# Kernel tuning notes

Measured on AMD Instinct MI355X. Metric: run time of the kernel, lower is better.

Reference implementation:

```python
import jax, jax.numpy as jnp
import numpy as np

N = 16384
INPUT_DIM = 256
HIDDEN1 = 128
HIDDEN2 = 64


def setup_inputs() -> dict:
    key = jax.random.key(0)
    ks = jax.random.split(key, 8)
    X = jax.random.normal(ks[0], (N, INPUT_DIM), dtype=jnp.float32)
    adj = jax.random.uniform(ks[1], (N, N), dtype=jnp.float32)
    # Xavier-uniform style scaling for weights
    def xavier(k, shape):
        fan_in, fan_out = shape
        lim = float(np.sqrt(6.0 / (fan_in + fan_out)))
        return jax.random.uniform(k, shape, dtype=jnp.float32, minval=-lim, maxval=lim)
    W1 = xavier(ks[2], (INPUT_DIM, HIDDEN1))
    Wm = xavier(ks[3], (HIDDEN1, HIDDEN2))
    Ws = xavier(ks[4], (HIDDEN1, HIDDEN2))
    Wp = xavier(ks[5], (HIDDEN2, HIDDEN2))
    bp = jnp.zeros((HIDDEN2,), dtype=jnp.float32)
    noise = jax.random.normal(ks[6], (N, HIDDEN2), dtype=jnp.float32)
    return {"X": X, "adj": adj, "W1": W1, "Wm": Wm, "Ws": Ws,
            "Wp": Wp, "bp": bp, "noise": noise}


def _gcn(x, adj, W, activation):
    # GraphConvSparse: adj @ (x @ W) then activation
    h = adj @ (x @ W)
    return activation(h)


def reference(X, adj, W1, Wm, Ws, Wp, bp, noise):
    # base GCN with ReLU
    hidden = _gcn(X, adj, W1, jax.nn.relu)            # [N, hidden1]
    # mean branch: identity-activation GCN then Linear projection
    Z = _gcn(hidden, adj, Wm, lambda x: x)            # [N, hidden2]
    mean = Z @ Wp + bp                                # [N, hidden2]
    # logstd branch with clamp(max=10)
    logstd = _gcn(hidden, adj, Ws, lambda x: x)
    logstd = jnp.minimum(logstd, 10.0)
    # reparameterization trick
    sampled_z = noise * jnp.exp(logstd) + mean        # [N, hidden2]
    return sampled_z
```

## Files before the change

kernel.cpp:

```cpp
#include <hip/hip_runtime.h>


typedef __bf16 bf16_t;
typedef __attribute__((ext_vector_type(8))) __bf16 bf16x8;
typedef __attribute__((ext_vector_type(16))) float f32x16;
typedef __attribute__((ext_vector_type(4)))  float f32x4;

#define N_NODES 16384

__device__ __forceinline__ int frag_off(int r, int c) {
    int K16  = r >> 4;
    int cblk = c >> 5;
    int g    = (r >> 3) & 1;
    int lane = (c & 31) + (g << 5);
    return ((K16 * 4 + cblk) << 9) + (lane << 3) + (r & 7);
}

template<int K, bool FUSED>
__global__ __launch_bounds__(256)
void producer_kernel(const float* __restrict__ A,
                     const float* __restrict__ W,
                     const float* __restrict__ Wa,
                     const float* __restrict__ Wb,
                     bf16_t* __restrict__ Bh,
                     bf16_t* __restrict__ Bl)
{
    __shared__ float As[32][128];
    __shared__ float Wsh[32][128];
    const int t    = threadIdx.x;
    const int row0 = blockIdx.x * 128;
    const int tc   = t & 15, tr = t >> 4;

    float acc[8][8];
    #pragma unroll
    for (int i = 0; i < 8; ++i)
        #pragma unroll
        for (int j = 0; j < 8; ++j) acc[i][j] = 0.f;

    const int ra = t >> 1, ks = (t & 1) << 4;
    const int wk = t >> 3, wc = (t & 7) << 4;

    for (int k0 = 0; k0 < K; k0 += 32) {
        const float* ap = A + (size_t)(row0 + ra) * K + k0 + ks;
        float4 a0 = *(const float4*)(ap);
        float4 a1 = *(const float4*)(ap + 4);
        float4 a2 = *(const float4*)(ap + 8);
        float4 a3 = *(const float4*)(ap + 12);
        float4 w0, w1, w2, w3;
        if (!FUSED) {
            const float* wp = W + (size_t)(k0 + wk) * 128 + wc;
            w0 = *(const float4*)(wp);     w1 = *(const float4*)(wp + 4);
            w2 = *(const float4*)(wp + 8); w3 = *(const float4*)(wp + 12);
        } else {
            const float* wp = (wc < 64) ? (Wa + (size_t)(k0 + wk) * 64 + wc)
                                        : (Wb + (size_t)(k0 + wk) * 64 + (wc - 64));
            w0 = *(const float4*)(wp);     w1 = *(const float4*)(wp + 4);
            w2 = *(const float4*)(wp + 8); w3 = *(const float4*)(wp + 12);
        }
        __syncthreads();
        {
            float tmp[16] = {a0.x,a0.y,a0.z,a0.w, a1.x,a1.y,a1.z,a1.w,
                             a2.x,a2.y,a2.z,a2.w, a3.x,a3.y,a3.z,a3.w};
            #pragma unroll
            for (int j = 0; j < 16; ++j) As[ks + j][ra] = tmp[j];
            *(float4*)&Wsh[wk][wc     ] = w0;
            *(float4*)&Wsh[wk][wc +  4] = w1;
            *(float4*)&Wsh[wk][wc +  8] = w2;
            *(float4*)&Wsh[wk][wc + 12] = w3;
        }
        __syncthreads();
        #pragma unroll 4
        for (int k = 0; k < 32; ++k) {
            float av[8], wv[8];
            *(float4*)&av[0] = *(const float4*)&As[k][8 * tr];
            *(float4*)&av[4] = *(const float4*)&As[k][8 * tr + 4];
            *(float4*)&wv[0] = *(const float4*)&Wsh[k][8 * tc];
            *(float4*)&wv[4] = *(const float4*)&Wsh[k][8 * tc + 4];
            #pragma unroll
            for (int i = 0; i < 8; ++i)
                #pragma unroll
                for (int j = 0; j < 8; ++j)
                    acc[i][j] = fmaf(av[i], wv[j], acc[i][j]);
        }
    }

    #pragma unroll
    for (int i = 0; i < 8; ++i) {
        int r = row0 + 8 * tr + i;
        #pragma unroll
        for (int j = 0; j < 8; ++j) {
            int c = 8 * tc + j;
            float v = acc[i][j];
            bf16_t h = (bf16_t)v;
            bf16_t l = (bf16_t)(v - (float)h);
            int off = frag_off(r, c);
            Bh[off] = h;
            Bl[off] = l;
        }
    }
}

template<int ACT>
__global__ __launch_bounds__(512, 2)
void adj_gemm_kernel(const float* __restrict__ adj,
                     const bf16_t* __restrict__ Bh,
                     const bf16_t* __restrict__ Bl,
                     float* __restrict__ out)
{
    __shared__ __align__(16) bf16_t AsH[2][64 * 64];
    __shared__ __align__(16) bf16_t AsL[2][64 * 64];
    const int t    = threadIdx.x;
    const int lane = t & 63;
    const int w    = t >> 6;
    const int wr   = w >> 2, wc = w & 3;
    const int row0 = blockIdx.x * 64;

    const int sr = t >> 3;
    const int sk = (t & 7) << 3;
    const float* aptr = adj + (size_t)(row0 + sr) * 16384 + sk;
    const int widx = ((sr << 6) + sk) ^ ((sr & 7) << 3);
    bf16_t* const wH0 = &AsH[0][widx]; bf16_t* const wH1 = &AsH[1][widx];
    bf16_t* const wL0 = &AsL[0][widx]; bf16_t* const wL1 = &AsL[1][widx];

    const int frow = (wr << 5) + (lane & 31);
    const int fg   = (lane >> 5) << 3;
    int ridx[4];
    #pragma unroll
    for (int s = 0; s < 4; ++s)
        ridx[s] = ((frow << 6) + (s << 4) + fg) ^ ((frow & 7) << 3);

    const int tb = (wc << 9) + (lane << 3);

    f32x16 acc;
    #pragma unroll
    for (int i = 0; i < 16; ++i) acc[i] = 0.f;

    auto loadB = [&](bf16x8* bh, bf16x8* bl, int step) {
        const size_t base = ((size_t)step << 13) + tb;
        #pragma unroll
        for (int s = 0; s < 4; ++s) {
            bh[s] = *(const bf16x8*)(Bh + base + (s << 11));
            bl[s] = *(const bf16x8*)(Bl + base + (s << 11));
        }
    };
    auto loadA = [&](f32x4& p0, f32x4& p1, int step) {
        const f32x4* p = (const f32x4*)(aptr + (step << 6));
        p0 = __builtin_nontemporal_load(p);
        p1 = __builtin_nontemporal_load(p + 1);
    };
    auto cvtWrite = [&](const f32x4& p0, const f32x4& p1, int buf) {
        float xs[8] = {p0[0], p0[1], p0[2], p0[3], p1[0], p1[1], p1[2], p1[3]};
        bf16x8 hv, lv;
        #pragma unroll
        for (int i = 0; i < 8; ++i) {
            bf16_t h = (bf16_t)xs[i];
            hv[i] = h;
            lv[i] = (bf16_t)(xs[i] - (float)h);
        }
        *(bf16x8*)(buf ? wH1 : wH0) = hv;
        *(bf16x8*)(buf ? wL1 : wL0) = lv;
    };
    auto compute = [&](int buf, const bf16x8* bh, const bf16x8* bl) {
        #pragma unroll
        for (int s = 0; s < 4; ++s) {
            const bf16_t* baseH = buf ? &AsH[1][0] : &AsH[0][0];
            const bf16_t* baseL = buf ? &AsL[1][0] : &AsL[0][0];
            bf16x8 ah = *(const bf16x8*)(baseH + ridx[s]);
            bf16x8 al = *(const bf16x8*)(baseL + ridx[s]);
            acc = __builtin_amdgcn_mfma_f32_32x32x16_bf16(ah, bh[s], acc, 0, 0, 0);
            acc = __builtin_amdgcn_mfma_f32_32x32x16_bf16(ah, bl[s], acc, 0, 0, 0);
            acc = __builtin_amdgcn_mfma_f32_32x32x16_bf16(al, bh[s], acc, 0, 0, 0);
        }
    };

#define SYNC_LDS() do { asm volatile("s_waitcnt lgkmcnt(0)" ::: "memory"); \
                        __builtin_amdgcn_s_barrier(); } while (0)

    f32x4 paA[4], paB[4];
    bf16x8 bhS0[4], blS0[4], bhS1[4], blS1[4];
    bf16x8 bhS2[4], blS2[4], bhS3[4], blS3[4];

    loadA(paA[0], paB[0], 0);
    loadA(paA[1], paB[1], 1);
    loadA(paA[2], paB[2], 2);
    loadA(paA[3], paB[3], 3);
    loadB(bhS0, blS0, 0);
    loadB(bhS1, blS1, 1);
    cvtWrite(paA[0], paB[0], 0);
    SYNC_LDS();

#define BODY(k, CH, CL, PH, PL) do {                                        \
        loadB(PH, PL, i0 + (k) + 2);                                        \
        loadA(paA[(k)], paB[(k)], i0 + (k) + 4);                            \
        compute((k) & 1, CH, CL);                                           \
        cvtWrite(paA[((k) + 1) & 3], paB[((k) + 1) & 3], ((k) + 1) & 1);    \
        SYNC_LDS();                                                         \
    } while (0)

    for (int i0 = 0; i0 < 252; i0 += 4) {
        BODY(0, bhS0, blS0, bhS2, blS2);
        BODY(1, bhS1, blS1, bhS3, blS3);
        BODY(2, bhS2, blS2, bhS0, blS0);
        BODY(3, bhS3, blS3, bhS1, blS1);
    }
#undef BODY

    loadB(bhS2, blS2, 254);
    compute(0, bhS0, blS0);
    cvtWrite(paA[1], paB[1], 1);
    SYNC_LDS();
    loadB(bhS3, blS3, 255);
    compute(1, bhS1, blS1);
    cvtWrite(paA[2], paB[2], 0);
    SYNC_LDS();
    compute(0, bhS2, blS2);
    cvtWrite(paA[3], paB[3], 1);
    SYNC_LDS();
    compute(1, bhS3, blS3);
#undef SYNC_LDS

    const int col = (wc << 5) + (lane & 31);
    const int rb  = row0 + (wr << 5) + ((lane >> 5) << 2);
    #pragma unroll
    for (int q = 0; q < 16; ++q) {
        int r = rb + (q & 3) + ((q >> 2) << 3);
        float v = acc[q];
        if (ACT == 1) v = fmaxf(v, 0.f);
        out[(size_t)r * 128 + col] = v;
    }
}

__global__ __launch_bounds__(256)
void final_kernel(const float* __restrict__ T,
                  const float* __restrict__ Wp,
                  const float* __restrict__ bp,
                  const float* __restrict__ noise,
                  float* __restrict__ out)
{
    __shared__ float Wps[64][64];
    __shared__ float Ts[64][64];
    const int t = threadIdx.x;
    const int row0 = blockIdx.x * 64;
    {
        int k = t >> 2, c0 = (t & 3) << 4;
        #pragma unroll
        for (int i = 0; i < 4; ++i)
            *(float4*)&Wps[k][c0 + 4 * i] = *(const float4*)&Wp[(size_t)k * 64 + c0 + 4 * i];
        #pragma unroll
        for (int i = 0; i < 4; ++i)
            *(float4*)&Ts[k][c0 + 4 * i] =
                *(const float4*)&T[(size_t)(row0 + k) * 128 + c0 + 4 * i];
    }
    __syncthreads();

    const int r  = t >> 2;
    const int c0 = (t & 3) << 4;
    float acc[16];
    #pragma unroll
    for (int j = 0; j < 16; ++j) acc[j] = bp[c0 + j];
    for (int k = 0; k < 64; ++k) {
        float a = Ts[r][k];
        #pragma unroll
        for (int j = 0; j < 16; ++j) acc[j] = fmaf(a, Wps[k][c0 + j], acc[j]);
    }
    const int grow = row0 + r;
    #pragma unroll
    for (int j = 0; j < 16; ++j) {
        float ls = T[(size_t)grow * 128 + 64 + c0 + j];
        ls = fminf(ls, 10.0f);
        out[(size_t)grow * 64 + c0 + j] =
            noise[(size_t)grow * 64 + c0 + j] * __expf(ls) + acc[j];
    }
}

extern "C" void kernel_launch(void* const* d_in, const int* in_sizes, int n_in,
                              void* d_out, int out_size, void* d_ws, size_t ws_size,
                              hipStream_t stream) {
    const float* X     = (const float*)d_in[0];
    const float* adj   = (const float*)d_in[1];
    const float* W1    = (const float*)d_in[2];
    const float* Wm    = (const float*)d_in[3];
    const float* Wsv   = (const float*)d_in[4];
    const float* Wp    = (const float*)d_in[5];
    const float* bp    = (const float*)d_in[6];
    const float* noise = (const float*)d_in[7];
    float* out = (float*)d_out;

    char* ws = (char*)d_ws;
    bf16_t* Bh   = (bf16_t*)ws;
    bf16_t* Bl   = (bf16_t*)(ws + (4u << 20));
    float*  Htmp = (float*)(ws + (8u << 20));

    producer_kernel<256, false><<<128, 256, 0, stream>>>(X, W1, nullptr, nullptr, Bh, Bl);
    adj_gemm_kernel<1><<<256, 512, 0, stream>>>(adj, Bh, Bl, Htmp);
    producer_kernel<128, true><<<128, 256, 0, stream>>>(Htmp, nullptr, Wm, Wsv, Bh, Bl);
    adj_gemm_kernel<0><<<256, 512, 0, stream>>>(adj, Bh, Bl, Htmp);
    final_kernel<<<256, 256, 0, stream>>>(Htmp, Wp, bp, noise, out);
}
```

Measured before the change: 783.1 us.

## Widen adjacency LDS tile to 256 K and cut barriers per tile

```diff
diff --git a/kernel.cpp b/kernel.cpp
--- a/kernel.cpp
+++ b/kernel.cpp
@@ -2,6 +2,7 @@
 
 
 typedef __bf16 bf16_t;
+typedef __attribute__((ext_vector_type(4))) __bf16 bf16x4;
 typedef __attribute__((ext_vector_type(8))) __bf16 bf16x8;
 typedef __attribute__((ext_vector_type(16))) float f32x16;
 typedef __attribute__((ext_vector_type(4)))  float f32x4;
@@ -107,27 +108,20 @@
                      const bf16_t* __restrict__ Bl,
                      float* __restrict__ out)
 {
-    __shared__ __align__(16) bf16_t AsH[2][64 * 64];
-    __shared__ __align__(16) bf16_t AsL[2][64 * 64];
+    __shared__ __align__(16) bf16_t AsH[2][64 * 256];
+    __shared__ __align__(16) bf16_t AsL[2][64 * 256];
     const int t    = threadIdx.x;
     const int lane = t & 63;
     const int w    = t >> 6;
     const int wr   = w >> 2, wc = w & 3;
     const int row0 = blockIdx.x * 64;
 
-    const int sr = t >> 3;
-    const int sk = (t & 7) << 3;
-    const float* aptr = adj + (size_t)(row0 + sr) * 16384 + sk;
-    const int widx = ((sr << 6) + sk) ^ ((sr & 7) << 3);
-    bf16_t* const wH0 = &AsH[0][widx]; bf16_t* const wH1 = &AsH[1][widx];
-    bf16_t* const wL0 = &AsL[0][widx]; bf16_t* const wL1 = &AsL[1][widx];
+    const float* aBase = adj + (size_t)(row0 + w * 8) * 16384 + lane * 4;
 
     const int frow = (wr << 5) + (lane & 31);
     const int fg   = (lane >> 5) << 3;
-    int ridx[4];
-    #pragma unroll
-    for (int s = 0; s < 4; ++s)
-        ridx[s] = ((frow << 6) + (s << 4) + fg) ^ ((frow & 7) << 3);
+    const int rswz = (frow & 7) << 3;
+    const int rbase = frow << 8;
 
     const int tb = (wc << 9) + (lane << 3);
 
@@ -135,38 +129,49 @@
     #pragma unroll
     for (int i = 0; i < 16; ++i) acc[i] = 0.f;
 
-    auto loadB = [&](bf16x8* bh, bf16x8* bl, int step) {
-        const size_t base = ((size_t)step << 13) + tb;
+    f32x4 ar[8];
+
+    auto loadAdj = [&](int mac) {
+        const float* p = aBase + (mac << 8);
+        ar[0] = __builtin_nontemporal_load((const f32x4*)(p));
+        ar[1] = __builtin_nontemporal_load((const f32x4*)(p + 16384));
+        ar[2] = __builtin_nontemporal_load((const f32x4*)(p + 2 * 16384));
+        ar[3] = __builtin_nontemporal_load((const f32x4*)(p + 3 * 16384));
+        ar[4] = __builtin_nontemporal_load((const f32x4*)(p + 4 * 16384));
+        ar[5] = __builtin_nontemporal_load((const f32x4*)(p + 5 * 16384));
+        ar[6] = __builtin_nontemporal_load((const f32x4*)(p + 6 * 16384));
+        ar[7] = __builtin_nontemporal_load((const f32x4*)(p + 7 * 16384));
+    };
+    auto cvtWrite = [&](int buf) {
+        #pragma unroll
+        for (int j = 0; j < 8; ++j) {
+            bf16x4 hv, lv;
+            #pragma unroll
+            for (int e = 0; e < 4; ++e) {
+                float v = ar[j][e];
+                bf16_t h = (bf16_t)v;
+                hv[e] = h;
+                lv[e] = (bf16_t)(v - (float)h);
+            }
+            int idx = (((w << 3) + j) << 8) + ((lane << 2) ^ (j << 3));
+            *(bf16x4*)&AsH[buf][idx] = hv;
+            *(bf16x4*)&AsL[buf][idx] = lv;
+        }
+    };
+    auto loadB = [&](bf16x8* bh, bf16x8* bl, int sub) {
+        const size_t base = ((size_t)sub << 13) + tb;
         #pragma unroll
         for (int s = 0; s < 4; ++s) {
             bh[s] = *(const bf16x8*)(Bh + base + (s << 11));
             bl[s] = *(const bf16x8*)(Bl + base + (s << 11));
         }
     };
-    auto loadA = [&](f32x4& p0, f32x4& p1, int step) {
-        const f32x4* p = (const f32x4*)(aptr + (step << 6));
-        p0 = __builtin_nontemporal_load(p);
-        p1 = __builtin_nontemporal_load(p + 1);
-    };
-    auto cvtWrite = [&](const f32x4& p0, const f32x4& p1, int buf) {
-        float xs[8] = {p0[0], p0[1], p0[2], p0[3], p1[0], p1[1], p1[2], p1[3]};
-        bf16x8 hv, lv;
-        #pragma unroll
-        for (int i = 0; i < 8; ++i) {
-            bf16_t h = (bf16_t)xs[i];
-            hv[i] = h;
-            lv[i] = (bf16_t)(xs[i] - (float)h);
-        }
-        *(bf16x8*)(buf ? wH1 : wH0) = hv;
-        *(bf16x8*)(buf ? wL1 : wL0) = lv;
-    };
-    auto compute = [&](int buf, const bf16x8* bh, const bf16x8* bl) {
+    auto compute = [&](int buf, const bf16x8* bh, const bf16x8* bl, int sbase) {
         #pragma unroll
         for (int s = 0; s < 4; ++s) {
-            const bf16_t* baseH = buf ? &AsH[1][0] : &AsH[0][0];
-            const bf16_t* baseL = buf ? &AsL[1][0] : &AsL[0][0];
-            bf16x8 ah = *(const bf16x8*)(baseH + ridx[s]);
-            bf16x8 al = *(const bf16x8*)(baseL + ridx[s]);
+            int idx = rbase + ((((sbase + s) << 4) + fg) ^ rswz);
+            bf16x8 ah = *(const bf16x8*)&AsH[buf][idx];
+            bf16x8 al = *(const bf16x8*)&AsL[buf][idx];
             acc = __builtin_amdgcn_mfma_f32_32x32x16_bf16(ah, bh[s], acc, 0, 0, 0);
             acc = __builtin_amdgcn_mfma_f32_32x32x16_bf16(ah, bl[s], acc, 0, 0, 0);
             acc = __builtin_amdgcn_mfma_f32_32x32x16_bf16(al, bh[s], acc, 0, 0, 0);
@@ -176,47 +181,37 @@
 #define SYNC_LDS() do { asm volatile("s_waitcnt lgkmcnt(0)" ::: "memory"); \
                         __builtin_amdgcn_s_barrier(); } while (0)
 
-    f32x4 paA[4], paB[4];
     bf16x8 bhS0[4], blS0[4], bhS1[4], blS1[4];
     bf16x8 bhS2[4], blS2[4], bhS3[4], blS3[4];
 
-    loadA(paA[0], paB[0], 0);
-    loadA(paA[1], paB[1], 1);
-    loadA(paA[2], paB[2], 2);
-    loadA(paA[3], paB[3], 3);
+    loadAdj(0);
+    cvtWrite(0);
     loadB(bhS0, blS0, 0);
     loadB(bhS1, blS1, 1);
-    cvtWrite(paA[0], paB[0], 0);
     SYNC_LDS();
-
-#define BODY(k, CH, CL, PH, PL) do {                                        \
-        loadB(PH, PL, i0 + (k) + 2);                                        \
-        loadA(paA[(k)], paB[(k)], i0 + (k) + 4);                            \
-        compute((k) & 1, CH, CL);                                           \
-        cvtWrite(paA[((k) + 1) & 3], paB[((k) + 1) & 3], ((k) + 1) & 1);    \
-        SYNC_LDS();                                                         \
-    } while (0)
-
-    for (int i0 = 0; i0 < 252; i0 += 4) {
-        BODY(0, bhS0, blS0, bhS2, blS2);
-        BODY(1, bhS1, blS1, bhS3, blS3);
-        BODY(2, bhS2, blS2, bhS0, blS0);
-        BODY(3, bhS3, blS3, bhS1, blS1);
-    }
-#undef BODY
-
+    loadAdj(1);
+
+    for (int m = 0; m < 63; ++m) {
+        const int buf = m & 1;
+        const int s4 = m << 2;
+        loadB(bhS2, blS2, s4 + 2);
+        compute(buf, bhS0, blS0, 0);
+        loadB(bhS3, blS3, s4 + 3);
+        compute(buf, bhS1, blS1, 4);
+        loadB(bhS0, blS0, s4 + 4);
+        cvtWrite(buf ^ 1);
+        compute(buf, bhS2, blS2, 8);
+        loadB(bhS1, blS1, s4 + 5);
+        compute(buf, bhS3, blS3, 12);
+        SYNC_LDS();
+        if (m < 62) loadAdj(m + 2);
+    }
     loadB(bhS2, blS2, 254);
-    compute(0, bhS0, blS0);
-    cvtWrite(paA[1], paB[1], 1);
-    SYNC_LDS();
+    compute(1, bhS0, blS0, 0);
     loadB(bhS3, blS3, 255);
-    compute(1, bhS1, blS1);
-    cvtWrite(paA[2], paB[2], 0);
-    SYNC_LDS();
-    compute(0, bhS2, blS2);
-    cvtWrite(paA[3], paB[3], 1);
-    SYNC_LDS();
-    compute(1, bhS3, blS3);
+    compute(1, bhS1, blS1, 4);
+    compute(1, bhS2, blS2, 8);
+    compute(1, bhS3, blS3, 12);
 #undef SYNC_LDS
 
     const int col = (wc << 5) + (lane & 31);
```

New measurement: 724.6 us. 7.5% less time.
